# Performance work log

Measured on AMD Instinct MI355X. Metric: run time of the kernel, lower is better.

The kernel has to match this reference:

```python
import jax, jax.numpy as jnp
import numpy as np

N = 50000      # nodes
E = 800000     # edges
G = 1024       # graphs in batch
D_IN = 9       # atom feature dim
D = 64         # embedding_size


def _lin(k, fan_in, shape):
    s = 1.0 / np.sqrt(fan_in)
    return jax.random.uniform(k, shape, jnp.float32, -s, s)


def setup_inputs() -> dict:
    key = jax.random.key(0)
    ks = jax.random.split(key, 12)
    x = jax.random.normal(ks[0], (N, D_IN), dtype=jnp.float32)
    edge_index = jax.random.randint(ks[1], (2, E), 0, N, dtype=jnp.int32)
    # node -> graph id, sorted, every graph non-empty
    batch = (jnp.arange(N) * G // N).astype(jnp.int32)
    W0 = _lin(ks[2], D_IN, (D_IN, D)); b0 = _lin(ks[3], D_IN, (D,))
    W1 = _lin(ks[4], D, (D, D));       b1 = _lin(ks[5], D, (D,))
    W2 = _lin(ks[6], D, (D, D));       b2 = _lin(ks[7], D, (D,))
    W3 = _lin(ks[8], D, (D, D));       b3 = _lin(ks[9], D, (D,))
    Wout = _lin(ks[10], 2 * D, (2 * D, 1)); bout = _lin(ks[11], 2 * D, (1,))
    return {"x": x, "edge_index": edge_index, "batch": batch,
            "W0": W0, "b0": b0, "W1": W1, "b1": b1,
            "W2": W2, "b2": b2, "W3": W3, "b3": b3,
            "Wout": Wout, "bout": bout}


def reference(x, edge_index, batch, W0, b0, W1, b1, W2, b2, W3, b3, Wout, bout):
    n = x.shape[0]
    # GCNConv: add self-loops, symmetric normalization D^-1/2 (A+I) D^-1/2
    loops = jnp.arange(n, dtype=edge_index.dtype)
    row = jnp.concatenate([edge_index[0], loops])  # source
    col = jnp.concatenate([edge_index[1], loops])  # destination
    deg = jax.ops.segment_sum(jnp.ones_like(col, dtype=x.dtype), col, num_segments=n)
    dinv = jax.lax.rsqrt(deg)  # deg >= 1 thanks to self-loops
    norm = dinv[row] * dinv[col]  # [E+N]

    def conv(h, W, b):
        h = h @ W                               # [N, D]
        msg = norm[:, None] * h[row]            # [E+N, D]
        return jax.ops.segment_sum(msg, col, num_segments=n) + b

    h = jnp.tanh(conv(x, W0, b0))
    h = jnp.tanh(conv(h, W1, b1))
    h = jnp.tanh(conv(h, W2, b2))
    h = jnp.tanh(conv(h, W3, b3))
    # dropout is identity in eval mode
    gmax = jax.ops.segment_max(h, batch, num_segments=G)                       # [G, D]
    cnt = jax.ops.segment_sum(jnp.ones((n, 1), h.dtype), batch, num_segments=G)
    gmean = jax.ops.segment_sum(h, batch, num_segments=G) / jnp.maximum(cnt, 1.0)
    pooled = jnp.concatenate([gmax, gmean], axis=1)                            # [G, 2D]
    return pooled @ Wout + bout
```

## Files before the change

### kernel.cpp

```cpp
#include <hip/hip_runtime.h>
#include <hip/hip_fp16.h>
#include <math.h>

#define N_NODES 50000
#define N_EDGES 800000
#define N_GRAPHS 1024
#define DIM 64
#define PAD 64
#define ZROW N_NODES
#define SLICE 6250
#define QBLK 208


__global__ void deg_fill(const int* __restrict__ row, const int* __restrict__ col,
                         int* __restrict__ ideg, int* __restrict__ esrc_pad) {
    int slice = blockIdx.x & 7;
    int q = blockIdx.x >> 3;
    int lo = slice * SLICE, hi = lo + SLICE;
    for (int e = q * 256 + threadIdx.x; e < N_EDGES; e += QBLK * 256) {
        int c = col[e];
        if (c >= lo && c < hi) {
            int rank = atomicAdd(&ideg[c], 1);
            if (rank < PAD) esrc_pad[c * PAD + rank] = row[e];
        }
    }
}


__global__ void gemm9(const float* __restrict__ x, const float* __restrict__ W,
                      const int* __restrict__ ideg, __half* __restrict__ th) {
    __shared__ float Wl[9 * DIM];
    int tid = threadIdx.x;
    for (int i = tid; i < 9 * DIM; i += 256) Wl[i] = W[i];
    __syncthreads();
    int node = blockIdx.x * 4 + (tid >> 6);
    int d = tid & 63;
    if (node >= N_NODES) return;
    const float* xr = x + (size_t)node * 9;
    float acc = 0.0f;
#pragma unroll
    for (int k = 0; k < 9; ++k) acc += xr[k] * Wl[k * DIM + d];
    float dv = rsqrtf((float)ideg[node] + 1.0f);
    th[(size_t)node * DIM + d] = __float2half(dv * acc);
}

__global__ void gemm64(const float* __restrict__ h, const float* __restrict__ W,
                       const int* __restrict__ ideg, uint2* __restrict__ th2) {
    __shared__ float At[64][68];
    __shared__ float Bl[64][68];
    int tid = threadIdx.x;
    int n0 = blockIdx.x * 64;

    {
        const float4* W4 = (const float4*)W;
#pragma unroll
        for (int i = 0; i < 4; ++i) {
            int idx = tid + 256 * i;
            int k = idx >> 4;
            int d4 = idx & 15;
            float4 v = W4[idx];
            *(float4*)&Bl[k][d4 * 4] = v;
        }
    }
    {
        int node = tid >> 2;
        int seg = tid & 3;
        int gn = n0 + node;
        bool ok = gn < N_NODES;
        const float4* h4 = (const float4*)h;
#pragma unroll
        for (int i = 0; i < 4; ++i) {
            int c4 = seg * 4 + i;
            float4 v = ok ? h4[(size_t)gn * 16 + c4] : make_float4(0.f, 0.f, 0.f, 0.f);
            int d = c4 * 4;
            At[d + 0][node] = v.x;
            At[d + 1][node] = v.y;
            At[d + 2][node] = v.z;
            At[d + 3][node] = v.w;
        }
    }
    __syncthreads();

    int ty = tid >> 4;
    int tx = tid & 15;
    float c00 = 0, c01 = 0, c02 = 0, c03 = 0;
    float c10 = 0, c11 = 0, c12 = 0, c13 = 0;
    float c20 = 0, c21 = 0, c22 = 0, c23 = 0;
    float c30 = 0, c31 = 0, c32 = 0, c33 = 0;
#pragma unroll 8
    for (int k = 0; k < 64; ++k) {
        float4 a = *(const float4*)&At[k][ty * 4];
        float4 b = *(const float4*)&Bl[k][tx * 4];
        c00 += a.x * b.x; c01 += a.x * b.y; c02 += a.x * b.z; c03 += a.x * b.w;
        c10 += a.y * b.x; c11 += a.y * b.y; c12 += a.y * b.z; c13 += a.y * b.w;
        c20 += a.z * b.x; c21 += a.z * b.y; c22 += a.z * b.z; c23 += a.z * b.w;
        c30 += a.w * b.x; c31 += a.w * b.y; c32 += a.w * b.z; c33 += a.w * b.w;
    }
    int gn = n0 + ty * 4;
#define STORE_ROW(r, CA, CB, CC, CD)                                          \
    if (gn + r < N_NODES) {                                                   \
        float dv = rsqrtf((float)ideg[gn + r] + 1.0f);                        \
        __half2 p0 = __floats2half2_rn(dv * CA, dv * CB);                     \
        __half2 p1 = __floats2half2_rn(dv * CC, dv * CD);                     \
        uint2 o;                                                              \
        o.x = *(unsigned*)&p0;                                                \
        o.y = *(unsigned*)&p1;                                                \
        th2[(size_t)(gn + r) * 16 + tx] = o;                                  \
    }
    STORE_ROW(0, c00, c01, c02, c03)
    STORE_ROW(1, c10, c11, c12, c13)
    STORE_ROW(2, c20, c21, c22, c23)
    STORE_ROW(3, c30, c31, c32, c33)
#undef STORE_ROW
}


__device__ __forceinline__ float4 h4tof4(uint2 v) {
    __half2 a = *reinterpret_cast<const __half2*>(&v.x);
    __half2 c = *reinterpret_cast<const __half2*>(&v.y);
    float2 fa = __half22float2(a);
    float2 fc = __half22float2(c);
    return make_float4(fa.x, fa.y, fc.x, fc.y);
}

__device__ __forceinline__ void add4(float4& a, const float4& r) {
    a.x += r.x; a.y += r.y; a.z += r.z; a.w += r.w;
}

__global__ void gather_tanh(const int* __restrict__ esrc_pad, const int* __restrict__ ideg,
                            const uint2* __restrict__ th2, const float* __restrict__ b,
                            float4* __restrict__ hout4) {
    int tid = threadIdx.x;
    int wid = tid >> 6;
    int lane = tid & 63;
    int sub = lane & 15;
    int grp = lane >> 4;
    int node = blockIdx.x * 16 + wid * 4 + grp;

    int deg = min(ideg[node], PAD);
    const int* ep = esrc_pad + node * PAD;

    float4 acc0 = h4tof4(th2[(size_t)node * 16 + sub]);
    float4 acc1 = make_float4(0.f, 0.f, 0.f, 0.f);
    float4 acc2 = make_float4(0.f, 0.f, 0.f, 0.f);
    float4 acc3 = make_float4(0.f, 0.f, 0.f, 0.f);

    for (int base = 0; base < deg; base += 16) {
        int4 i0 = *(const int4*)(ep + base + 0);
        int4 i1 = *(const int4*)(ep + base + 4);
        int4 i2 = *(const int4*)(ep + base + 8);
        int4 i3 = *(const int4*)(ep + base + 12);
        int idx[16] = {i0.x, i0.y, i0.z, i0.w, i1.x, i1.y, i1.z, i1.w,
                       i2.x, i2.y, i2.z, i2.w, i3.x, i3.y, i3.z, i3.w};
        int rem = deg - base;
        uint2 r[16];
#pragma unroll
        for (int j = 0; j < 16; ++j) {
            int s = (j < rem) ? idx[j] : ZROW;
            r[j] = th2[(size_t)s * 16 + sub];
        }
#pragma unroll
        for (int j = 0; j < 16; ++j) {
            float4 v = h4tof4(r[j]);
            if ((j & 3) == 0) add4(acc0, v);
            else if ((j & 3) == 1) add4(acc1, v);
            else if ((j & 3) == 2) add4(acc2, v);
            else add4(acc3, v);
        }
    }

    float4 acc;
    acc.x = (acc0.x + acc1.x) + (acc2.x + acc3.x);
    acc.y = (acc0.y + acc1.y) + (acc2.y + acc3.y);
    acc.z = (acc0.z + acc1.z) + (acc2.z + acc3.z);
    acc.w = (acc0.w + acc1.w) + (acc2.w + acc3.w);

    float4 bv = ((const float4*)b)[sub];
    float dv = rsqrtf((float)deg + 1.0f);
    float4 res;
    res.x = tanhf(dv * acc.x + bv.x);
    res.y = tanhf(dv * acc.y + bv.y);
    res.z = tanhf(dv * acc.z + bv.z);
    res.w = tanhf(dv * acc.w + bv.w);
    hout4[(size_t)node * 16 + sub] = res;
}


__device__ __forceinline__ int lower_bound(const int* a, int n, int key) {
    int lo = 0, hi = n;
    while (lo < hi) {
        int mid = (lo + hi) >> 1;
        if (a[mid] < key) lo = mid + 1; else hi = mid;
    }
    return lo;
}

__global__ void pool_out(const float* __restrict__ h, const int* __restrict__ batch,
                         const float* __restrict__ Wout, const float* __restrict__ bout,
                         float* __restrict__ out) {
    __shared__ float smax[4][DIM];
    __shared__ float ssum[4][DIM];
    __shared__ int bounds[2];
    int g = blockIdx.x;
    int tid = threadIdx.x, w = tid >> 6, d = tid & 63;
    if (tid == 0) {
        bounds[0] = lower_bound(batch, N_NODES, g);
        bounds[1] = lower_bound(batch, N_NODES, g + 1);
    }
    __syncthreads();
    int start = bounds[0], end = bounds[1];
    float mx = -INFINITY, sum = 0.0f;
    for (int n = start + w; n < end; n += 4) {
        float v = h[(size_t)n * DIM + d];
        mx = fmaxf(mx, v);
        sum += v;
    }
    smax[w][d] = mx;
    ssum[w][d] = sum;
    __syncthreads();
    if (w == 0) {
        mx = fmaxf(fmaxf(smax[0][d], smax[1][d]), fmaxf(smax[2][d], smax[3][d]));
        sum = ssum[0][d] + ssum[1][d] + ssum[2][d] + ssum[3][d];
        float cnt = (float)(end - start);
        float mean = sum / fmaxf(cnt, 1.0f);
        float v = mx * Wout[d] + mean * Wout[DIM + d];
#pragma unroll
        for (int off = 32; off > 0; off >>= 1) v += __shfl_down(v, off, 64);
        if (d == 0) out[g] = v + bout[0];
    }
}


static inline size_t align256(size_t x) { return (x + 255) & ~(size_t)255; }

extern "C" void kernel_launch(void* const* d_in, const int* in_sizes, int n_in,
                              void* d_out, int out_size, void* d_ws, size_t ws_size,
                              hipStream_t stream) {
    const float* x     = (const float*)d_in[0];
    const int*   ei    = (const int*)d_in[1];
    const int*   batch = (const int*)d_in[2];
    const float* W0    = (const float*)d_in[3];
    const float* b0    = (const float*)d_in[4];
    const float* W1    = (const float*)d_in[5];
    const float* b1    = (const float*)d_in[6];
    const float* W2    = (const float*)d_in[7];
    const float* b2    = (const float*)d_in[8];
    const float* W3    = (const float*)d_in[9];
    const float* b3    = (const float*)d_in[10];
    const float* Wout  = (const float*)d_in[11];
    const float* bout  = (const float*)d_in[12];
    float* out = (float*)d_out;

    const int* row = ei;
    const int* col = ei + N_EDGES;

    char* ws = (char*)d_ws;
    size_t off = 0;
    int*    ideg     = (int*)(ws + off);    off += align256((size_t)N_NODES * 4);
    int*    esrc_pad = (int*)(ws + off);    off += align256((size_t)N_NODES * PAD * 4);
    __half* th       = (__half*)(ws + off); off += align256(((size_t)N_NODES + 1) * DIM * 2);
    float*  hA       = (float*)(ws + off);  off += align256((size_t)N_NODES * DIM * 4);
    (void)ws_size;

    const int wave_blocks = N_NODES / 4;
    const int gath_blocks = N_NODES / 16;
    const int gemm_blocks = (N_NODES + 63) / 64;

    hipMemsetAsync(ideg, 0, (size_t)N_NODES * 4, stream);
    hipMemsetAsync(th + (size_t)ZROW * DIM, 0, DIM * 2, stream);
    deg_fill<<<8 * QBLK, 256, 0, stream>>>(row, col, ideg, esrc_pad);

    gemm9<<<wave_blocks, 256, 0, stream>>>(x, W0, ideg, th);
    gather_tanh<<<gath_blocks, 256, 0, stream>>>(esrc_pad, ideg, (const uint2*)th, b0, (float4*)hA);

    const float* Ws[3] = {W1, W2, W3};
    const float* bs[3] = {b1, b2, b3};
    for (int l = 0; l < 3; ++l) {
        gemm64<<<gemm_blocks, 256, 0, stream>>>(hA, Ws[l], ideg, (uint2*)th);
        gather_tanh<<<gath_blocks, 256, 0, stream>>>(esrc_pad, ideg, (const uint2*)th, bs[l], (float4*)hA);
    }

    pool_out<<<N_GRAPHS, 256, 0, stream>>>(hA, batch, Wout, bout, out);
    (void)out_size; (void)n_in; (void)in_sizes;
}
```

Measured before the change: 273.9 us.

## Split fp16 feature table into two 32-column planes and gather per plane

Stores the scaled fp16 node features as two planes of 32 columns each, and runs the gather/tanh kernel twice per layer, once per plane, with each lane handling 2 columns. This halves the working set each gather pass touches so it fits better in L2/MALL, in exchange for re-reading the edge index lists twice and launching twice as many gather kernels. It also adds nontemporal loads and stores on streaming data (edge lists, hidden activations) so they do not evict the feature table from cache.

```diff
diff --git a/kernel.cpp b/kernel.cpp
--- a/kernel.cpp
+++ b/kernel.cpp
@@ -11,6 +11,25 @@
 #define SLICE 6250
 #define QBLK 208
 
+#define PLANE ((size_t)(N_NODES + 1) * 32)
+
+typedef int   v4i __attribute__((ext_vector_type(4)));
+typedef float v2f __attribute__((ext_vector_type(2)));
+typedef float v4f __attribute__((ext_vector_type(4)));
+
+__device__ __forceinline__ int4 ntld4i(const int* p) {
+    v4i v = __builtin_nontemporal_load((const v4i*)p);
+    return make_int4(v[0], v[1], v[2], v[3]);
+}
+__device__ __forceinline__ float4 ntld4f(const float* p) {
+    v4f v = __builtin_nontemporal_load((const v4f*)p);
+    return make_float4(v[0], v[1], v[2], v[3]);
+}
+__device__ __forceinline__ void ntst2f(float2* p, float x, float y) {
+    v2f v; v[0] = x; v[1] = y;
+    __builtin_nontemporal_store(v, (v2f*)p);
+}
+
 
 __global__ void deg_fill(const int* __restrict__ row, const int* __restrict__ col,
                          int* __restrict__ ideg, int* __restrict__ esrc_pad) {
@@ -18,10 +37,10 @@
     int q = blockIdx.x >> 3;
     int lo = slice * SLICE, hi = lo + SLICE;
     for (int e = q * 256 + threadIdx.x; e < N_EDGES; e += QBLK * 256) {
-        int c = col[e];
+        int c = __builtin_nontemporal_load(col + e);
         if (c >= lo && c < hi) {
             int rank = atomicAdd(&ideg[c], 1);
-            if (rank < PAD) esrc_pad[c * PAD + rank] = row[e];
+            if (rank < PAD) esrc_pad[c * PAD + rank] = __builtin_nontemporal_load(row + e);
         }
     }
 }
@@ -41,11 +60,11 @@
 #pragma unroll
     for (int k = 0; k < 9; ++k) acc += xr[k] * Wl[k * DIM + d];
     float dv = rsqrtf((float)ideg[node] + 1.0f);
-    th[(size_t)node * DIM + d] = __float2half(dv * acc);
+    th[(size_t)(d >> 5) * PLANE + (size_t)node * 32 + (d & 31)] = __float2half(dv * acc);
 }
 
 __global__ void gemm64(const float* __restrict__ h, const float* __restrict__ W,
-                       const int* __restrict__ ideg, uint2* __restrict__ th2) {
+                       const int* __restrict__ ideg, __half* __restrict__ th) {
     __shared__ float At[64][68];
     __shared__ float Bl[64][68];
     int tid = threadIdx.x;
@@ -67,11 +86,11 @@
         int seg = tid & 3;
         int gn = n0 + node;
         bool ok = gn < N_NODES;
-        const float4* h4 = (const float4*)h;
 #pragma unroll
         for (int i = 0; i < 4; ++i) {
             int c4 = seg * 4 + i;
-            float4 v = ok ? h4[(size_t)gn * 16 + c4] : make_float4(0.f, 0.f, 0.f, 0.f);
+            float4 v = ok ? ntld4f(h + (size_t)gn * 64 + c4 * 4)
+                          : make_float4(0.f, 0.f, 0.f, 0.f);
             int d = c4 * 4;
             At[d + 0][node] = v.x;
             At[d + 1][node] = v.y;
@@ -97,6 +116,8 @@
         c30 += a.w * b.x; c31 += a.w * b.y; c32 += a.w * b.z; c33 += a.w * b.w;
     }
     int gn = n0 + ty * 4;
+    uint2* tp = (uint2*)(th + (size_t)(tx >> 3) * PLANE);
+    int txl = tx & 7;
 #define STORE_ROW(r, CA, CB, CC, CD)                                          \
     if (gn + r < N_NODES) {                                                   \
         float dv = rsqrtf((float)ideg[gn + r] + 1.0f);                        \
@@ -105,7 +126,7 @@
         uint2 o;                                                              \
         o.x = *(unsigned*)&p0;                                                \
         o.y = *(unsigned*)&p1;                                                \
-        th2[(size_t)(gn + r) * 16 + tx] = o;                                  \
+        tp[(size_t)(gn + r) * 8 + txl] = o;                                   \
     }
     STORE_ROW(0, c00, c01, c02, c03)
     STORE_ROW(1, c10, c11, c12, c13)
@@ -115,21 +136,14 @@
 }
 
 
-__device__ __forceinline__ float4 h4tof4(uint2 v) {
-    __half2 a = *reinterpret_cast<const __half2*>(&v.x);
-    __half2 c = *reinterpret_cast<const __half2*>(&v.y);
-    float2 fa = __half22float2(a);
-    float2 fc = __half22float2(c);
-    return make_float4(fa.x, fa.y, fc.x, fc.y);
-}
-
-__device__ __forceinline__ void add4(float4& a, const float4& r) {
-    a.x += r.x; a.y += r.y; a.z += r.z; a.w += r.w;
+__device__ __forceinline__ float2 h2tof2(unsigned u) {
+    __half2 h = *reinterpret_cast<const __half2*>(&u);
+    return __half22float2(h);
 }
 
 __global__ void gather_tanh(const int* __restrict__ esrc_pad, const int* __restrict__ ideg,
-                            const uint2* __restrict__ th2, const float* __restrict__ b,
-                            float4* __restrict__ hout4) {
+                            const unsigned* __restrict__ thp, const float* __restrict__ b,
+                            const int pass, float2* __restrict__ hout2) {
     int tid = threadIdx.x;
     int wid = tid >> 6;
     int lane = tid & 63;
@@ -140,49 +154,43 @@
     int deg = min(ideg[node], PAD);
     const int* ep = esrc_pad + node * PAD;
 
-    float4 acc0 = h4tof4(th2[(size_t)node * 16 + sub]);
-    float4 acc1 = make_float4(0.f, 0.f, 0.f, 0.f);
-    float4 acc2 = make_float4(0.f, 0.f, 0.f, 0.f);
-    float4 acc3 = make_float4(0.f, 0.f, 0.f, 0.f);
+    float2 acc0 = h2tof2(thp[(size_t)node * 16 + sub]);
+    float2 acc1 = make_float2(0.f, 0.f);
+    float2 acc2 = make_float2(0.f, 0.f);
+    float2 acc3 = make_float2(0.f, 0.f);
 
     for (int base = 0; base < deg; base += 16) {
-        int4 i0 = *(const int4*)(ep + base + 0);
-        int4 i1 = *(const int4*)(ep + base + 4);
-        int4 i2 = *(const int4*)(ep + base + 8);
-        int4 i3 = *(const int4*)(ep + base + 12);
+        int4 i0 = ntld4i(ep + base + 0);
+        int4 i1 = ntld4i(ep + base + 4);
+        int4 i2 = ntld4i(ep + base + 8);
+        int4 i3 = ntld4i(ep + base + 12);
         int idx[16] = {i0.x, i0.y, i0.z, i0.w, i1.x, i1.y, i1.z, i1.w,
                        i2.x, i2.y, i2.z, i2.w, i3.x, i3.y, i3.z, i3.w};
         int rem = deg - base;
-        uint2 r[16];
+        unsigned r[16];
 #pragma unroll
         for (int j = 0; j < 16; ++j) {
             int s = (j < rem) ? idx[j] : ZROW;
-            r[j] = th2[(size_t)s * 16 + sub];
+            r[j] = thp[(size_t)s * 16 + sub];
         }
 #pragma unroll
         for (int j = 0; j < 16; ++j) {
-            float4 v = h4tof4(r[j]);
-            if ((j & 3) == 0) add4(acc0, v);
-            else if ((j & 3) == 1) add4(acc1, v);
-            else if ((j & 3) == 2) add4(acc2, v);
-            else add4(acc3, v);
-        }
-    }
-
-    float4 acc;
-    acc.x = (acc0.x + acc1.x) + (acc2.x + acc3.x);
-    acc.y = (acc0.y + acc1.y) + (acc2.y + acc3.y);
-    acc.z = (acc0.z + acc1.z) + (acc2.z + acc3.z);
-    acc.w = (acc0.w + acc1.w) + (acc2.w + acc3.w);
-
-    float4 bv = ((const float4*)b)[sub];
+            float2 v = h2tof2(r[j]);
+            if ((j & 3) == 0)      { acc0.x += v.x; acc0.y += v.y; }
+            else if ((j & 3) == 1) { acc1.x += v.x; acc1.y += v.y; }
+            else if ((j & 3) == 2) { acc2.x += v.x; acc2.y += v.y; }
+            else                   { acc3.x += v.x; acc3.y += v.y; }
+        }
+    }
+
+    float ax = (acc0.x + acc1.x) + (acc2.x + acc3.x);
+    float ay = (acc0.y + acc1.y) + (acc2.y + acc3.y);
+
+    float2 bv = ((const float2*)b)[pass * 16 + sub];
     float dv = rsqrtf((float)deg + 1.0f);
-    float4 res;
-    res.x = tanhf(dv * acc.x + bv.x);
-    res.y = tanhf(dv * acc.y + bv.y);
-    res.z = tanhf(dv * acc.z + bv.z);
-    res.w = tanhf(dv * acc.w + bv.w);
-    hout4[(size_t)node * 16 + sub] = res;
+    float rx = tanhf(dv * ax + bv.x);
+    float ry = tanhf(dv * ay + bv.y);
+    ntst2f(&hout2[(size_t)node * 32 + pass * 16 + sub], rx, ry);
 }
 
 
@@ -211,7 +219,7 @@
     int start = bounds[0], end = bounds[1];
     float mx = -INFINITY, sum = 0.0f;
     for (int n = start + w; n < end; n += 4) {
-        float v = h[(size_t)n * DIM + d];
+        float v = __builtin_nontemporal_load(h + (size_t)n * DIM + d);
         mx = fmaxf(mx, v);
         sum += v;
     }
@@ -258,7 +266,7 @@
     size_t off = 0;
     int*    ideg     = (int*)(ws + off);    off += align256((size_t)N_NODES * 4);
     int*    esrc_pad = (int*)(ws + off);    off += align256((size_t)N_NODES * PAD * 4);
-    __half* th       = (__half*)(ws + off); off += align256(((size_t)N_NODES + 1) * DIM * 2);
+    __half* th       = (__half*)(ws + off); off += align256(2 * PLANE * 2);
     float*  hA       = (float*)(ws + off);  off += align256((size_t)N_NODES * DIM * 4);
     (void)ws_size;
 
@@ -267,17 +275,22 @@
     const int gemm_blocks = (N_NODES + 63) / 64;
 
     hipMemsetAsync(ideg, 0, (size_t)N_NODES * 4, stream);
-    hipMemsetAsync(th + (size_t)ZROW * DIM, 0, DIM * 2, stream);
+    hipMemsetAsync(th + (size_t)ZROW * 32, 0, 32 * 2, stream);
+    hipMemsetAsync(th + PLANE + (size_t)ZROW * 32, 0, 32 * 2, stream);
     deg_fill<<<8 * QBLK, 256, 0, stream>>>(row, col, ideg, esrc_pad);
 
     gemm9<<<wave_blocks, 256, 0, stream>>>(x, W0, ideg, th);
-    gather_tanh<<<gath_blocks, 256, 0, stream>>>(esrc_pad, ideg, (const uint2*)th, b0, (float4*)hA);
+    for (int p = 0; p < 2; ++p)
+        gather_tanh<<<gath_blocks, 256, 0, stream>>>(
+            esrc_pad, ideg, (const unsigned*)(th + (size_t)p * PLANE), b0, p, (float2*)hA);
 
     const float* Ws[3] = {W1, W2, W3};
     const float* bs[3] = {b1, b2, b3};
     for (int l = 0; l < 3; ++l) {
-        gemm64<<<gemm_blocks, 256, 0, stream>>>(hA, Ws[l], ideg, (uint2*)th);
-        gather_tanh<<<gath_blocks, 256, 0, stream>>>(esrc_pad, ideg, (const uint2*)th, bs[l], (float4*)hA);
+        gemm64<<<gemm_blocks, 256, 0, stream>>>(hA, Ws[l], ideg, th);
+        for (int p = 0; p < 2; ++p)
+            gather_tanh<<<gath_blocks, 256, 0, stream>>>(
+                esrc_pad, ideg, (const unsigned*)(th + (size_t)p * PLANE), bs[l], p, (float2*)hA);
     }
 
     pool_out<<<N_GRAPHS, 256, 0, stream>>>(hA, batch, Wout, bout, out);
```

After: 313.1 us. 14.3% more time.

## Split neighbor gather by source-node half to shrink per-pass gather working set

Applied to the files above, without the earlier changes.

Edges are bucketed by whether the source node is in the lower or upper half of the node range, giving two padded adjacency lists and two degree counters. Each layer's gather then runs as two passes: the first accumulates lower-half sources into an fp32 partial buffer, and the second adds upper-half sources and applies the bias and tanh. The aim is to halve the gathered feature table each pass touches so it fits better in cache. Nontemporal loads and stores are added for streaming buffers. The cost is an extra kernel launch per layer, a full fp32 partial write and read, and doubled index padding memory.

```diff
diff --git a/kernel.cpp b/kernel.cpp
--- a/kernel.cpp
+++ b/kernel.cpp
@@ -7,28 +7,53 @@
 #define N_GRAPHS 1024
 #define DIM 64
 #define PAD 64
+#define HALF_N 25000
 #define ZROW N_NODES
 #define SLICE 6250
 #define QBLK 208
 
+typedef int   v4i __attribute__((ext_vector_type(4)));
+typedef float v4f __attribute__((ext_vector_type(4)));
+
+__device__ __forceinline__ int4 ntld4i(const int* p) {
+    v4i v = __builtin_nontemporal_load((const v4i*)p);
+    return make_int4(v[0], v[1], v[2], v[3]);
+}
+__device__ __forceinline__ float4 ntld4f(const float* p) {
+    v4f v = __builtin_nontemporal_load((const v4f*)p);
+    return make_float4(v[0], v[1], v[2], v[3]);
+}
+__device__ __forceinline__ void ntst4f(float4* p, float4 v) {
+    v4f w; w[0] = v.x; w[1] = v.y; w[2] = v.z; w[3] = v.w;
+    __builtin_nontemporal_store(w, (v4f*)p);
+}
+
 
 __global__ void deg_fill(const int* __restrict__ row, const int* __restrict__ col,
-                         int* __restrict__ ideg, int* __restrict__ esrc_pad) {
+                         int* __restrict__ ideg_lo, int* __restrict__ ideg_hi,
+                         int* __restrict__ esrc_lo, int* __restrict__ esrc_hi) {
     int slice = blockIdx.x & 7;
     int q = blockIdx.x >> 3;
     int lo = slice * SLICE, hi = lo + SLICE;
     for (int e = q * 256 + threadIdx.x; e < N_EDGES; e += QBLK * 256) {
-        int c = col[e];
+        int c = __builtin_nontemporal_load(col + e);
         if (c >= lo && c < hi) {
-            int rank = atomicAdd(&ideg[c], 1);
-            if (rank < PAD) esrc_pad[c * PAD + rank] = row[e];
+            int r = __builtin_nontemporal_load(row + e);
+            if (r < HALF_N) {
+                int rank = atomicAdd(&ideg_lo[c], 1);
+                if (rank < PAD) esrc_lo[c * PAD + rank] = r;
+            } else {
+                int rank = atomicAdd(&ideg_hi[c], 1);
+                if (rank < PAD) esrc_hi[c * PAD + rank] = r;
+            }
         }
     }
 }
 
 
 __global__ void gemm9(const float* __restrict__ x, const float* __restrict__ W,
-                      const int* __restrict__ ideg, __half* __restrict__ th) {
+                      const int* __restrict__ ideg_lo, const int* __restrict__ ideg_hi,
+                      __half* __restrict__ th) {
     __shared__ float Wl[9 * DIM];
     int tid = threadIdx.x;
     for (int i = tid; i < 9 * DIM; i += 256) Wl[i] = W[i];
@@ -40,12 +65,13 @@
     float acc = 0.0f;
 #pragma unroll
     for (int k = 0; k < 9; ++k) acc += xr[k] * Wl[k * DIM + d];
-    float dv = rsqrtf((float)ideg[node] + 1.0f);
+    float dv = rsqrtf((float)(ideg_lo[node] + ideg_hi[node]) + 1.0f);
     th[(size_t)node * DIM + d] = __float2half(dv * acc);
 }
 
 __global__ void gemm64(const float* __restrict__ h, const float* __restrict__ W,
-                       const int* __restrict__ ideg, uint2* __restrict__ th2) {
+                       const int* __restrict__ ideg_lo, const int* __restrict__ ideg_hi,
+                       uint2* __restrict__ th2) {
     __shared__ float At[64][68];
     __shared__ float Bl[64][68];
     int tid = threadIdx.x;
@@ -67,11 +93,11 @@
         int seg = tid & 3;
         int gn = n0 + node;
         bool ok = gn < N_NODES;
-        const float4* h4 = (const float4*)h;
 #pragma unroll
         for (int i = 0; i < 4; ++i) {
             int c4 = seg * 4 + i;
-            float4 v = ok ? h4[(size_t)gn * 16 + c4] : make_float4(0.f, 0.f, 0.f, 0.f);
+            float4 v = ok ? ntld4f(h + (size_t)gn * 64 + c4 * 4)
+                          : make_float4(0.f, 0.f, 0.f, 0.f);
             int d = c4 * 4;
             At[d + 0][node] = v.x;
             At[d + 1][node] = v.y;
@@ -99,7 +125,7 @@
     int gn = n0 + ty * 4;
 #define STORE_ROW(r, CA, CB, CC, CD)                                          \
     if (gn + r < N_NODES) {                                                   \
-        float dv = rsqrtf((float)ideg[gn + r] + 1.0f);                        \
+        float dv = rsqrtf((float)(ideg_lo[gn + r] + ideg_hi[gn + r]) + 1.0f); \
         __half2 p0 = __floats2half2_rn(dv * CA, dv * CB);                     \
         __half2 p1 = __floats2half2_rn(dv * CC, dv * CD);                     \
         uint2 o;                                                              \
@@ -127,9 +153,8 @@
     a.x += r.x; a.y += r.y; a.z += r.z; a.w += r.w;
 }
 
-__global__ void gather_tanh(const int* __restrict__ esrc_pad, const int* __restrict__ ideg,
-                            const uint2* __restrict__ th2, const float* __restrict__ b,
-                            float4* __restrict__ hout4) {
+__global__ void gather_lo(const int* __restrict__ esrc, const int* __restrict__ ideg_lo,
+                          const uint2* __restrict__ th2, float4* __restrict__ hP) {
     int tid = threadIdx.x;
     int wid = tid >> 6;
     int lane = tid & 63;
@@ -137,19 +162,20 @@
     int grp = lane >> 4;
     int node = blockIdx.x * 16 + wid * 4 + grp;
 
-    int deg = min(ideg[node], PAD);
-    const int* ep = esrc_pad + node * PAD;
-
-    float4 acc0 = h4tof4(th2[(size_t)node * 16 + sub]);
+    int deg = min(ideg_lo[node], PAD);
+    const int* ep = esrc + node * PAD;
+
+    float4 acc0 = (node < HALF_N) ? h4tof4(th2[(size_t)node * 16 + sub])
+                                  : make_float4(0.f, 0.f, 0.f, 0.f);
     float4 acc1 = make_float4(0.f, 0.f, 0.f, 0.f);
     float4 acc2 = make_float4(0.f, 0.f, 0.f, 0.f);
     float4 acc3 = make_float4(0.f, 0.f, 0.f, 0.f);
 
     for (int base = 0; base < deg; base += 16) {
-        int4 i0 = *(const int4*)(ep + base + 0);
-        int4 i1 = *(const int4*)(ep + base + 4);
-        int4 i2 = *(const int4*)(ep + base + 8);
-        int4 i3 = *(const int4*)(ep + base + 12);
+        int4 i0 = ntld4i(ep + base + 0);
+        int4 i1 = ntld4i(ep + base + 4);
+        int4 i2 = ntld4i(ep + base + 8);
+        int4 i3 = ntld4i(ep + base + 12);
         int idx[16] = {i0.x, i0.y, i0.z, i0.w, i1.x, i1.y, i1.z, i1.w,
                        i2.x, i2.y, i2.z, i2.w, i3.x, i3.y, i3.z, i3.w};
         int rem = deg - base;
@@ -174,15 +200,68 @@
     acc.y = (acc0.y + acc1.y) + (acc2.y + acc3.y);
     acc.z = (acc0.z + acc1.z) + (acc2.z + acc3.z);
     acc.w = (acc0.w + acc1.w) + (acc2.w + acc3.w);
+    ntst4f(&hP[(size_t)node * 16 + sub], acc);
+}
+
+__global__ void gather_hi(const int* __restrict__ esrc, const int* __restrict__ ideg_lo,
+                          const int* __restrict__ ideg_hi, const uint2* __restrict__ th2,
+                          const float4* __restrict__ hP, const float* __restrict__ b,
+                          float4* __restrict__ hout4) {
+    int tid = threadIdx.x;
+    int wid = tid >> 6;
+    int lane = tid & 63;
+    int sub = lane & 15;
+    int grp = lane >> 4;
+    int node = blockIdx.x * 16 + wid * 4 + grp;
+
+    int dlo = min(ideg_lo[node], PAD);
+    int deg = min(ideg_hi[node], PAD);
+    const int* ep = esrc + node * PAD;
+
+    float4 acc0 = ntld4f((const float*)&hP[(size_t)node * 16 + sub]);
+    if (node >= HALF_N) add4(acc0, h4tof4(th2[(size_t)node * 16 + sub]));
+    float4 acc1 = make_float4(0.f, 0.f, 0.f, 0.f);
+    float4 acc2 = make_float4(0.f, 0.f, 0.f, 0.f);
+    float4 acc3 = make_float4(0.f, 0.f, 0.f, 0.f);
+
+    for (int base = 0; base < deg; base += 16) {
+        int4 i0 = ntld4i(ep + base + 0);
+        int4 i1 = ntld4i(ep + base + 4);
+        int4 i2 = ntld4i(ep + base + 8);
+        int4 i3 = ntld4i(ep + base + 12);
+        int idx[16] = {i0.x, i0.y, i0.z, i0.w, i1.x, i1.y, i1.z, i1.w,
+                       i2.x, i2.y, i2.z, i2.w, i3.x, i3.y, i3.z, i3.w};
+        int rem = deg - base;
+        uint2 r[16];
+#pragma unroll
+        for (int j = 0; j < 16; ++j) {
+            int s = (j < rem) ? idx[j] : ZROW;
+            r[j] = th2[(size_t)s * 16 + sub];
+        }
+#pragma unroll
+        for (int j = 0; j < 16; ++j) {
+            float4 v = h4tof4(r[j]);
+            if ((j & 3) == 0) add4(acc0, v);
+            else if ((j & 3) == 1) add4(acc1, v);
+            else if ((j & 3) == 2) add4(acc2, v);
+            else add4(acc3, v);
+        }
+    }
+
+    float4 acc;
+    acc.x = (acc0.x + acc1.x) + (acc2.x + acc3.x);
+    acc.y = (acc0.y + acc1.y) + (acc2.y + acc3.y);
+    acc.z = (acc0.z + acc1.z) + (acc2.z + acc3.z);
+    acc.w = (acc0.w + acc1.w) + (acc2.w + acc3.w);
 
     float4 bv = ((const float4*)b)[sub];
-    float dv = rsqrtf((float)deg + 1.0f);
+    float dv = rsqrtf((float)(dlo + deg) + 1.0f);
     float4 res;
     res.x = tanhf(dv * acc.x + bv.x);
     res.y = tanhf(dv * acc.y + bv.y);
     res.z = tanhf(dv * acc.z + bv.z);
     res.w = tanhf(dv * acc.w + bv.w);
-    hout4[(size_t)node * 16 + sub] = res;
+    ntst4f(&hout4[(size_t)node * 16 + sub], res);
 }
 
 
@@ -211,7 +290,7 @@
     int start = bounds[0], end = bounds[1];
     float mx = -INFINITY, sum = 0.0f;
     for (int n = start + w; n < end; n += 4) {
-        float v = h[(size_t)n * DIM + d];
+        float v = __builtin_nontemporal_load(h + (size_t)n * DIM + d);
         mx = fmaxf(mx, v);
         sum += v;
     }
@@ -256,28 +335,36 @@
 
     char* ws = (char*)d_ws;
     size_t off = 0;
-    int*    ideg     = (int*)(ws + off);    off += align256((size_t)N_NODES * 4);
-    int*    esrc_pad = (int*)(ws + off);    off += align256((size_t)N_NODES * PAD * 4);
+    int*    ideg     = (int*)(ws + off);    off += align256((size_t)N_NODES * 2 * 4);
+    int*    esrc_lo  = (int*)(ws + off);    off += align256((size_t)N_NODES * PAD * 4);
+    int*    esrc_hi  = (int*)(ws + off);    off += align256((size_t)N_NODES * PAD * 4);
     __half* th       = (__half*)(ws + off); off += align256(((size_t)N_NODES + 1) * DIM * 2);
     float*  hA       = (float*)(ws + off);  off += align256((size_t)N_NODES * DIM * 4);
+    float*  hP       = (float*)(ws + off);  off += align256((size_t)N_NODES * DIM * 4);
     (void)ws_size;
+    int* ideg_lo = ideg;
+    int* ideg_hi = ideg + N_NODES;
 
     const int wave_blocks = N_NODES / 4;
     const int gath_blocks = N_NODES / 16;
     const int gemm_blocks = (N_NODES + 63) / 64;
 
-    hipMemsetAsync(ideg, 0, (size_t)N_NODES * 4, stream);
+    hipMemsetAsync(ideg, 0, (size_t)N_NODES * 2 * 4, stream);
     hipMemsetAsync(th + (size_t)ZROW * DIM, 0, DIM * 2, stream);
-    deg_fill<<<8 * QBLK, 256, 0, stream>>>(row, col, ideg, esrc_pad);
-
-    gemm9<<<wave_blocks, 256, 0, stream>>>(x, W0, ideg, th);
-    gather_tanh<<<gath_blocks, 256, 0, stream>>>(esrc_pad, ideg, (const uint2*)th, b0, (float4*)hA);
+    deg_fill<<<8 * QBLK, 256, 0, stream>>>(row, col, ideg_lo, ideg_hi, esrc_lo, esrc_hi);
+
+    gemm9<<<wave_blocks, 256, 0, stream>>>(x, W0, ideg_lo, ideg_hi, th);
+    gather_lo<<<gath_blocks, 256, 0, stream>>>(esrc_lo, ideg_lo, (const uint2*)th, (float4*)hP);
+    gather_hi<<<gath_blocks, 256, 0, stream>>>(esrc_hi, ideg_lo, ideg_hi, (const uint2*)th,
+                                               (const float4*)hP, b0, (float4*)hA);
 
     const float* Ws[3] = {W1, W2, W3};
     const float* bs[3] = {b1, b2, b3};
     for (int l = 0; l < 3; ++l) {
-        gemm64<<<gemm_blocks, 256, 0, stream>>>(hA, Ws[l], ideg, (uint2*)th);
-        gather_tanh<<<gath_blocks, 256, 0, stream>>>(esrc_pad, ideg, (const uint2*)th, bs[l], (float4*)hA);
+        gemm64<<<gemm_blocks, 256, 0, stream>>>(hA, Ws[l], ideg_lo, ideg_hi, (uint2*)th);
+        gather_lo<<<gath_blocks, 256, 0, stream>>>(esrc_lo, ideg_lo, (const uint2*)th, (float4*)hP);
+        gather_hi<<<gath_blocks, 256, 0, stream>>>(esrc_hi, ideg_lo, ideg_hi, (const uint2*)th,
+                                                   (const float4*)hP, bs[l], (float4*)hA);
     }
 
     pool_out<<<N_GRAPHS, 256, 0, stream>>>(hA, batch, Wout, bout, out);
```

Result: slower. 322.6 us (+17.8%).

## Compact edge indices to 16-bit, single-pass CSR fill, nontemporal hints

Applied to the files above, without the earlier changes.

Stores padded per-node source indices as unsigned short instead of int. This halves the index array footprint and the index traffic in every gather layer. The old slice-partitioned degree/fill kernel read the edge list eight times; it is replaced by one pass where each thread takes four edges using vectorized loads and direct atomics. Nontemporal loads and stores are added for streaming activations in gemm64, gather_tanh output and pooling. The 16-bit indices only work while the node count stays below 65536, and the unsliced atomics lose the L2 locality the slicing provided.

```diff
diff --git a/kernel.cpp b/kernel.cpp
--- a/kernel.cpp
+++ b/kernel.cpp
@@ -8,22 +8,38 @@
 #define DIM 64
 #define PAD 64
 #define ZROW N_NODES
-#define SLICE 6250
-#define QBLK 208
-
-
-__global__ void deg_fill(const int* __restrict__ row, const int* __restrict__ col,
-                         int* __restrict__ ideg, int* __restrict__ esrc_pad) {
-    int slice = blockIdx.x & 7;
-    int q = blockIdx.x >> 3;
-    int lo = slice * SLICE, hi = lo + SLICE;
-    for (int e = q * 256 + threadIdx.x; e < N_EDGES; e += QBLK * 256) {
-        int c = col[e];
-        if (c >= lo && c < hi) {
-            int rank = atomicAdd(&ideg[c], 1);
-            if (rank < PAD) esrc_pad[c * PAD + rank] = row[e];
-        }
-    }
+
+typedef int   v4i __attribute__((ext_vector_type(4)));
+typedef float v4f __attribute__((ext_vector_type(4)));
+
+__device__ __forceinline__ int4 ntld4i(const int* p) {
+    v4i v = __builtin_nontemporal_load((const v4i*)p);
+    return make_int4(v[0], v[1], v[2], v[3]);
+}
+__device__ __forceinline__ float4 ntld4f(const float* p) {
+    v4f v = __builtin_nontemporal_load((const v4f*)p);
+    return make_float4(v[0], v[1], v[2], v[3]);
+}
+__device__ __forceinline__ void ntst4f(float4* p, float4 v) {
+    v4f w; w[0] = v.x; w[1] = v.y; w[2] = v.z; w[3] = v.w;
+    __builtin_nontemporal_store(w, (v4f*)p);
+}
+
+
+__global__ void fill_csr(const int* __restrict__ row, const int* __restrict__ col,
+                         int* __restrict__ ideg, unsigned short* __restrict__ esrc) {
+    int t = blockIdx.x * 256 + threadIdx.x;
+    if (t >= N_EDGES / 4) return;
+    int4 c = ntld4i(col + t * 4);
+    int4 r = ntld4i(row + t * 4);
+    int k0 = atomicAdd(&ideg[c.x], 1);
+    int k1 = atomicAdd(&ideg[c.y], 1);
+    int k2 = atomicAdd(&ideg[c.z], 1);
+    int k3 = atomicAdd(&ideg[c.w], 1);
+    if (k0 < PAD) esrc[c.x * PAD + k0] = (unsigned short)r.x;
+    if (k1 < PAD) esrc[c.y * PAD + k1] = (unsigned short)r.y;
+    if (k2 < PAD) esrc[c.z * PAD + k2] = (unsigned short)r.z;
+    if (k3 < PAD) esrc[c.w * PAD + k3] = (unsigned short)r.w;
 }
 
 
@@ -67,11 +83,11 @@
         int seg = tid & 3;
         int gn = n0 + node;
         bool ok = gn < N_NODES;
-        const float4* h4 = (const float4*)h;
 #pragma unroll
         for (int i = 0; i < 4; ++i) {
             int c4 = seg * 4 + i;
-            float4 v = ok ? h4[(size_t)gn * 16 + c4] : make_float4(0.f, 0.f, 0.f, 0.f);
+            float4 v = ok ? ntld4f(h + (size_t)gn * 64 + c4 * 4)
+                          : make_float4(0.f, 0.f, 0.f, 0.f);
             int d = c4 * 4;
             At[d + 0][node] = v.x;
             At[d + 1][node] = v.y;
@@ -127,7 +143,7 @@
     a.x += r.x; a.y += r.y; a.z += r.z; a.w += r.w;
 }
 
-__global__ void gather_tanh(const int* __restrict__ esrc_pad, const int* __restrict__ ideg,
+__global__ void gather_tanh(const unsigned short* __restrict__ esrc, const int* __restrict__ ideg,
                             const uint2* __restrict__ th2, const float* __restrict__ b,
                             float4* __restrict__ hout4) {
     int tid = threadIdx.x;
@@ -138,7 +154,7 @@
     int node = blockIdx.x * 16 + wid * 4 + grp;
 
     int deg = min(ideg[node], PAD);
-    const int* ep = esrc_pad + node * PAD;
+    const uint4* ep4 = (const uint4*)(esrc + node * PAD);
 
     float4 acc0 = h4tof4(th2[(size_t)node * 16 + sub]);
     float4 acc1 = make_float4(0.f, 0.f, 0.f, 0.f);
@@ -146,12 +162,15 @@
     float4 acc3 = make_float4(0.f, 0.f, 0.f, 0.f);
 
     for (int base = 0; base < deg; base += 16) {
-        int4 i0 = *(const int4*)(ep + base + 0);
-        int4 i1 = *(const int4*)(ep + base + 4);
-        int4 i2 = *(const int4*)(ep + base + 8);
-        int4 i3 = *(const int4*)(ep + base + 12);
-        int idx[16] = {i0.x, i0.y, i0.z, i0.w, i1.x, i1.y, i1.z, i1.w,
-                       i2.x, i2.y, i2.z, i2.w, i3.x, i3.y, i3.z, i3.w};
+        uint4 u0 = ep4[(base >> 3) + 0];
+        uint4 u1 = ep4[(base >> 3) + 1];
+        unsigned w[8] = {u0.x, u0.y, u0.z, u0.w, u1.x, u1.y, u1.z, u1.w};
+        int idx[16];
+#pragma unroll
+        for (int j = 0; j < 8; ++j) {
+            idx[2 * j + 0] = (int)(w[j] & 0xffffu);
+            idx[2 * j + 1] = (int)(w[j] >> 16);
+        }
         int rem = deg - base;
         uint2 r[16];
 #pragma unroll
@@ -182,7 +201,7 @@
     res.y = tanhf(dv * acc.y + bv.y);
     res.z = tanhf(dv * acc.z + bv.z);
     res.w = tanhf(dv * acc.w + bv.w);
-    hout4[(size_t)node * 16 + sub] = res;
+    ntst4f(&hout4[(size_t)node * 16 + sub], res);
 }
 
 
@@ -211,7 +230,7 @@
     int start = bounds[0], end = bounds[1];
     float mx = -INFINITY, sum = 0.0f;
     for (int n = start + w; n < end; n += 4) {
-        float v = h[(size_t)n * DIM + d];
+        float v = __builtin_nontemporal_load(h + (size_t)n * DIM + d);
         mx = fmaxf(mx, v);
         sum += v;
     }
@@ -256,28 +275,29 @@
 
     char* ws = (char*)d_ws;
     size_t off = 0;
-    int*    ideg     = (int*)(ws + off);    off += align256((size_t)N_NODES * 4);
-    int*    esrc_pad = (int*)(ws + off);    off += align256((size_t)N_NODES * PAD * 4);
-    __half* th       = (__half*)(ws + off); off += align256(((size_t)N_NODES + 1) * DIM * 2);
-    float*  hA       = (float*)(ws + off);  off += align256((size_t)N_NODES * DIM * 4);
+    int*            ideg = (int*)(ws + off);            off += align256((size_t)N_NODES * 4);
+    unsigned short* esrc = (unsigned short*)(ws + off); off += align256((size_t)N_NODES * PAD * 2);
+    __half*         th   = (__half*)(ws + off);         off += align256(((size_t)N_NODES + 1) * DIM * 2);
+    float*          hA   = (float*)(ws + off);          off += align256((size_t)N_NODES * DIM * 4);
     (void)ws_size;
 
+    const int fill_blocks = (N_EDGES / 4 + 255) / 256;
     const int wave_blocks = N_NODES / 4;
     const int gath_blocks = N_NODES / 16;
     const int gemm_blocks = (N_NODES + 63) / 64;
 
     hipMemsetAsync(ideg, 0, (size_t)N_NODES * 4, stream);
     hipMemsetAsync(th + (size_t)ZROW * DIM, 0, DIM * 2, stream);
-    deg_fill<<<8 * QBLK, 256, 0, stream>>>(row, col, ideg, esrc_pad);
+    fill_csr<<<fill_blocks, 256, 0, stream>>>(row, col, ideg, esrc);
 
     gemm9<<<wave_blocks, 256, 0, stream>>>(x, W0, ideg, th);
-    gather_tanh<<<gath_blocks, 256, 0, stream>>>(esrc_pad, ideg, (const uint2*)th, b0, (float4*)hA);
+    gather_tanh<<<gath_blocks, 256, 0, stream>>>(esrc, ideg, (const uint2*)th, b0, (float4*)hA);
 
     const float* Ws[3] = {W1, W2, W3};
     const float* bs[3] = {b1, b2, b3};
     for (int l = 0; l < 3; ++l) {
         gemm64<<<gemm_blocks, 256, 0, stream>>>(hA, Ws[l], ideg, (uint2*)th);
-        gather_tanh<<<gath_blocks, 256, 0, stream>>>(esrc_pad, ideg, (const uint2*)th, bs[l], (float4*)hA);
+        gather_tanh<<<gath_blocks, 256, 0, stream>>>(esrc, ideg, (const uint2*)th, bs[l], (float4*)hA);
     }
 
     pool_out<<<N_GRAPHS, 256, 0, stream>>>(hA, batch, Wout, bout, out);
```

Measured after the change: 291.0 us. +6.2%, slower.
